# Performance work log

Measured on AMD Instinct MI355X. Metric: run time of the kernel, lower is better.

## Reference

```python
import jax, jax.numpy as jnp
import numpy as np

D_MODEL = 512
NUM_HEADS = 8
D_K = D_MODEL // NUM_HEADS  # 64
LN_EPS = 1e-5


def setup_inputs() -> dict:
    key = jax.random.key(0)
    ks = jax.random.split(key, 6)
    B, S, D = 8, 1024, D_MODEL
    scale = 1.0 / np.sqrt(D)
    return {
        "query": jax.random.normal(ks[0], (B, S, D), jnp.float32),
        "key": jax.random.normal(ks[1], (B, S, D), jnp.float32),
        "value": jax.random.normal(ks[2], (B, S, D), jnp.float32),
        "Wq": jax.random.normal(ks[3], (D, D), jnp.float32) * scale,
        "bq": jnp.zeros((D,), jnp.float32),
        "Wk": jax.random.normal(ks[4], (D, D), jnp.float32) * scale,
        "bk": jnp.zeros((D,), jnp.float32),
        "Wo": jax.random.normal(ks[5], (D, D * NUM_HEADS), jnp.float32) * (1.0 / np.sqrt(D * NUM_HEADS)),
        "bo": jnp.zeros((D,), jnp.float32),
        "gamma": jnp.ones((D,), jnp.float32),
        "beta": jnp.zeros((D,), jnp.float32),
    }


def reference(query, key, value, Wq, bq, Wk, bk, Wo, bo, gamma, beta):
    B, S, D = value.shape
    h, dk = NUM_HEADS, D_K
    # QK projections -> [B, h, S, dk]
    q = (query @ Wq.T + bq).reshape(B, S, h, dk).transpose(0, 2, 1, 3)
    k = (key @ Wk.T + bk).reshape(B, S, h, dk).transpose(0, 2, 1, 3)
    # scaled dot-product scores [B, h, Sq, Sk]
    scores = jnp.einsum("bhqd,bhkd->bhqk", q, k) / jnp.sqrt(jnp.asarray(dk, q.dtype))
    attn = jax.nn.softmax(scores, axis=-1)
    # value broadcast across heads: value is [B, Sk, D] -> per-head output [B, h, Sq, D]
    x = jnp.einsum("bhqk,bkd->bhqd", attn, value)
    # concat heads -> [B, Sq, h*D], output projection back to D
    x = x.transpose(0, 2, 1, 3).reshape(B, S, h * D)
    x = x @ Wo.T + bo
    # residual + LayerNorm (dropout = identity in eval)
    y = value + x
    mu = jnp.mean(y, axis=-1, keepdims=True)
    var = jnp.var(y, axis=-1, keepdims=True)
    out = (y - mu) * jax.lax.rsqrt(var + LN_EPS) * gamma + beta
    return out, attn
```

## Files before the change

kernel.cpp:

```cpp
#include <hip/hip_runtime.h>
#include <hip/hip_bf16.h>

#define B_ 8
#define S_ 1024
#define D_ 512
#define H_ 8
#define DK_ 64
#define HD_ 4096

typedef __attribute__((ext_vector_type(8))) short bf16x8;
typedef __attribute__((ext_vector_type(4))) float f32x4;

static __device__ __forceinline__ unsigned short f2bf(float f) {
    unsigned u = __float_as_uint(f);
    unsigned r = (u + 0x7fffu + ((u >> 16) & 1u)) >> 16;
    return (unsigned short)r;
}

static __device__ __forceinline__ void gload16(const unsigned short* g, unsigned short* l) {
    __builtin_amdgcn_global_load_lds(
        (const __attribute__((address_space(1))) void*)g,
        (__attribute__((address_space(3))) void*)l, 16, 0, 0);
}

static __device__ __forceinline__ int plidx(int ql, int k) {
    return ql * 1024 + ((((k >> 3) ^ (ql & 7))) << 3) + (k & 7);
}

__global__ __launch_bounds__(256) void cvt_kernel(
    const float* __restrict__ src, unsigned short* __restrict__ dst)
{
    const size_t i = ((size_t)blockIdx.x * 256 + threadIdx.x) * 4;
    float4 v = *(const float4*)&src[i];
    ushort4 u = { f2bf(v.x), f2bf(v.y), f2bf(v.z), f2bf(v.w) };
    *(ushort4*)&dst[i] = u;
}

__global__ __launch_bounds__(256) void vt_kernel(
    const float* __restrict__ V, unsigned short* __restrict__ Vt)
{
    __shared__ float tile[32][33];
    const int b = blockIdx.z, s0 = blockIdx.x * 32, e0 = blockIdx.y * 32;
    const int t = threadIdx.x;
    const int r = t >> 3, c4 = (t & 7) * 4;
    float4 v = *(const float4*)&V[((size_t)b * S_ + s0 + r) * D_ + e0 + c4];
    tile[r][c4 + 0] = v.x; tile[r][c4 + 1] = v.y;
    tile[r][c4 + 2] = v.z; tile[r][c4 + 3] = v.w;
    __syncthreads();
    ushort4 u;
    u.x = f2bf(tile[c4 + 0][r]); u.y = f2bf(tile[c4 + 1][r]);
    u.z = f2bf(tile[c4 + 2][r]); u.w = f2bf(tile[c4 + 3][r]);
    *(ushort4*)&Vt[((size_t)b * D_ + e0 + r) * S_ + s0 + c4] = u;
}

template<int KDIM, int MODE>
__global__ __launch_bounds__(256) void gemm128(
    const unsigned short* __restrict__ A, const unsigned short* __restrict__ Bw,
    const float* __restrict__ bias, const float* __restrict__ Vres,
    void* __restrict__ Out, float scale)
{
    const int o = blockIdx.x;
    const int nb = (o & 7) * 32 + (o >> 3);
    const int m0 = (nb >> 2) * 128;
    const int n0 = (nb & 3) * 128;

    __shared__ __align__(16) unsigned short As[2][128 * 32];
    __shared__ __align__(16) unsigned short Bs[2][128 * 32];

    const int t = threadIdx.x;
    const int wave = t >> 6, lane = t & 63;
    const int wr = wave >> 1, wc = wave & 1;
    const int lr = lane & 15, g = lane >> 4;
    const int gx = (g ^ (lr & 3)) << 3;

    f32x4 acc[4][4];
    #pragma unroll
    for (int r = 0; r < 4; ++r)
        #pragma unroll
        for (int c = 0; c < 4; ++c) acc[r][c] = (f32x4){0.f, 0.f, 0.f, 0.f};

    const int sub = lane >> 2;
    const int cb  = (((lane & 3) ^ (sub & 3)) << 3);

    auto stage = [&](int buf, int k0) {
        #pragma unroll
        for (int s = 0; s < 2; ++s) {
            const int chunk = s * 4 + wave;
            const int row = chunk * 16 + sub;
            gload16(&A [(size_t)(m0 + row) * KDIM + k0 + cb], &As[buf][chunk * 512]);
            gload16(&Bw[(size_t)(n0 + row) * KDIM + k0 + cb], &Bs[buf][chunk * 512]);
        }
    };
    auto compute = [&](int cur) {
        bf16x8 af[4], bfr[4];
        #pragma unroll
        for (int r = 0; r < 4; ++r)
            af[r] = *(const bf16x8*)&As[cur][(wr * 64 + r * 16 + lr) * 32 + gx];
        #pragma unroll
        for (int c = 0; c < 4; ++c)
            bfr[c] = *(const bf16x8*)&Bs[cur][(wc * 64 + c * 16 + lr) * 32 + gx];
        #pragma unroll
        for (int c = 0; c < 4; ++c)
            #pragma unroll
            for (int r = 0; r < 4; ++r)
                acc[r][c] = __builtin_amdgcn_mfma_f32_16x16x32_bf16(af[r], bfr[c], acc[r][c], 0, 0, 0);
    };

    const int NT = KDIM / 32;
    stage(0, 0);
    __syncthreads();
    int cur = 0;
    for (int tt = 0; tt < NT - 1; ++tt) {
        stage(cur ^ 1, (tt + 1) * 32);
        compute(cur);
        __syncthreads();
        cur ^= 1;
    }
    compute(cur);

    float bn[4];
    #pragma unroll
    for (int c = 0; c < 4; ++c) bn[c] = bias[n0 + wc * 64 + c * 16 + lr];

    #pragma unroll
    for (int r = 0; r < 4; ++r) {
        #pragma unroll
        for (int c = 0; c < 4; ++c) {
            const int n = n0 + wc * 64 + c * 16 + lr;
            #pragma unroll
            for (int i = 0; i < 4; ++i) {
                const int m = m0 + wr * 64 + r * 16 + g * 4 + i;
                if constexpr (MODE == 0) {
                    const int srow = m & 1023, bb = m >> 10;
                    const int h = n >> 6, dk = n & 63;
                    ((unsigned short*)Out)[(((size_t)(bb * H_ + h)) * S_ + srow) * DK_ + dk] =
                        f2bf((acc[r][c][i] + bn[c]) * scale);
                } else {
                    const size_t oo = (size_t)m * D_ + n;
                    ((float*)Out)[oo] = acc[r][c][i] + bn[c] + Vres[oo];
                }
            }
        }
    }
}

__global__ __launch_bounds__(1024, 4) void fused_attn(
    const unsigned short* __restrict__ Qbf,
    const unsigned short* __restrict__ Kbf,
    const unsigned short* __restrict__ Vt,
    float* __restrict__ attn,
    unsigned short* __restrict__ AV)
{
    const int bh = blockIdx.y;
    const int b = bh >> 3, h = bh & 7;
    const int q0 = blockIdx.x * 64;
    const unsigned short* Qb = Qbf + (size_t)bh * S_ * DK_;
    const unsigned short* Kb = Kbf + (size_t)bh * S_ * DK_;
    const unsigned short* Vb = Vt + (size_t)b * D_ * S_;
    float* outp = attn + ((size_t)bh << 20);

    __shared__ unsigned short PL[64 * 1024];
    __shared__ float redm[64][16];
    __shared__ float rowm[64];

    const int t = threadIdx.x;
    const int wave = t >> 6, lane = t & 63;
    const int wcol = wave * 64;
    const int lr = lane & 15;
    const int g  = lane >> 4;

    f32x4 acc[4][4];
    #pragma unroll
    for (int r = 0; r < 4; ++r)
        #pragma unroll
        for (int c = 0; c < 4; ++c) acc[r][c] = (f32x4){0.f, 0.f, 0.f, 0.f};

    #pragma unroll
    for (int kk = 0; kk < 2; ++kk) {
        bf16x8 af[4];
        #pragma unroll
        for (int r = 0; r < 4; ++r)
            af[r] = *(const bf16x8*)&Kb[(size_t)(wcol + r * 16 + lr) * DK_ + kk * 32 + g * 8];
        bf16x8 qf[4];
        #pragma unroll
        for (int c = 0; c < 4; ++c)
            qf[c] = *(const bf16x8*)&Qb[(size_t)(q0 + c * 16 + lr) * DK_ + kk * 32 + g * 8];
        #pragma unroll
        for (int r = 0; r < 4; ++r)
            #pragma unroll
            for (int c = 0; c < 4; ++c)
                acc[r][c] = __builtin_amdgcn_mfma_f32_16x16x32_bf16(af[r], qf[c], acc[r][c], 0, 0, 0);
    }

    float mloc[4];
    #pragma unroll
    for (int c = 0; c < 4; ++c) {
        float m = acc[0][c][0];
        #pragma unroll
        for (int r = 0; r < 4; ++r)
            #pragma unroll
            for (int i = 0; i < 4; ++i) m = fmaxf(m, acc[r][c][i]);
        m = fmaxf(m, __shfl_xor(m, 16));
        m = fmaxf(m, __shfl_xor(m, 32));
        mloc[c] = m;
    }
    if (lane < 16) {
        #pragma unroll
        for (int c = 0; c < 4; ++c) redm[c * 16 + lane][wave] = mloc[c];
    }
    __syncthreads();
    if (t < 64) {
        float m = redm[t][0];
        #pragma unroll
        for (int w = 1; w < 16; ++w) m = fmaxf(m, redm[t][w]);
        rowm[t] = m;
    }
    __syncthreads();
    float sloc[4];
    #pragma unroll
    for (int c = 0; c < 4; ++c) {
        const float m = rowm[c * 16 + lr];
        float s = 0.f;
        #pragma unroll
        for (int r = 0; r < 4; ++r)
            #pragma unroll
            for (int i = 0; i < 4; ++i) {
                float p = __expf(acc[r][c][i] - m);
                acc[r][c][i] = p;
                s += p;
            }
        s += __shfl_xor(s, 16);
        s += __shfl_xor(s, 32);
        sloc[c] = s;
    }
    if (lane < 16) {
        #pragma unroll
        for (int c = 0; c < 4; ++c) redm[c * 16 + lane][wave] = sloc[c];
    }
    __syncthreads();
    if (t < 64) {
        float s = redm[t][0];
        #pragma unroll
        for (int w = 1; w < 16; ++w) s += redm[t][w];
        rowm[t] = 1.0f / s;
    }
    __syncthreads();

    #pragma unroll
    for (int c = 0; c < 4; ++c) {
        const int ql = c * 16 + lr;
        const float ri = rowm[ql];
        #pragma unroll
        for (int r = 0; r < 4; ++r) {
            f32x4 v = acc[r][c];
            v[0] *= ri; v[1] *= ri; v[2] *= ri; v[3] *= ri;
            const int k = wcol + r * 16 + g * 4;
            unsigned p01 = (unsigned)f2bf(v[0]) | ((unsigned)f2bf(v[1]) << 16);
            unsigned p23 = (unsigned)f2bf(v[2]) | ((unsigned)f2bf(v[3]) << 16);
            uint2 pk = { p01, p23 };
            *(uint2*)&PL[plidx(ql, k)] = pk;
        }
    }
    __syncthreads();

    const int we = wave * 32;
    f32x4 accv[4][2];
    #pragma unroll
    for (int r = 0; r < 4; ++r)
        #pragma unroll
        for (int c = 0; c < 2; ++c) accv[r][c] = (f32x4){0.f, 0.f, 0.f, 0.f};

    for (int k0 = 0; k0 < S_; k0 += 32) {
        bf16x8 pa[4];
        #pragma unroll
        for (int r = 0; r < 4; ++r)
            pa[r] = *(const bf16x8*)&PL[plidx(r * 16 + lr, k0 + g * 8)];
        #pragma unroll
        for (int c = 0; c < 2; ++c) {
            const int e = we + c * 16 + lr;
            bf16x8 vf = *(const bf16x8*)&Vb[(size_t)e * S_ + k0 + g * 8];
            #pragma unroll
            for (int r = 0; r < 4; ++r)
                accv[r][c] = __builtin_amdgcn_mfma_f32_16x16x32_bf16(pa[r], vf, accv[r][c], 0, 0, 0);
        }
    }

    {
        const int arow = t >> 4;
        const int akb  = (t & 15) * 8;
        float* rowp = outp + ((size_t)(q0 + arow) << 10);
        #pragma unroll
        for (int j = 0; j < 8; ++j) {
            const int k = akb + j * 128;
            uint4 u = *(const uint4*)&PL[plidx(arow, k)];
            float4 f0, f1;
            f0.x = __uint_as_float((u.x & 0xffffu) << 16);
            f0.y = __uint_as_float(u.x & 0xffff0000u);
            f0.z = __uint_as_float((u.y & 0xffffu) << 16);
            f0.w = __uint_as_float(u.y & 0xffff0000u);
            f1.x = __uint_as_float((u.z & 0xffffu) << 16);
            f1.y = __uint_as_float(u.z & 0xffff0000u);
            f1.z = __uint_as_float((u.w & 0xffffu) << 16);
            f1.w = __uint_as_float(u.w & 0xffff0000u);
            *(float4*)&rowp[k] = f0;
            *(float4*)&rowp[k + 4] = f1;
        }
    }
    __syncthreads();

    unsigned short* PLs = PL;
    #pragma unroll
    for (int r = 0; r < 4; ++r)
        #pragma unroll
        for (int c = 0; c < 2; ++c) {
            const int e = we + c * 16 + lr;
            #pragma unroll
            for (int i = 0; i < 4; ++i) {
                const int q = r * 16 + g * 4 + i;
                PLs[q * 512 + (e ^ ((q & 7) << 3))] = f2bf(accv[r][c][i]);
            }
        }
    __syncthreads();
    {
        const int row = t >> 4;
        unsigned short* avp = AV + ((size_t)(b * S_ + q0 + row)) * HD_ + h * D_;
        #pragma unroll
        for (int j = 0; j < 4; ++j) {
            const int e0 = (t & 15) * 8 + j * 128;
            uint4 u = *(const uint4*)&PLs[row * 512 + (e0 ^ ((row & 7) << 3))];
            *(uint4*)&avp[e0] = u;
        }
    }
}

__global__ __launch_bounds__(256) void ln_kernel(
    float* __restrict__ Y, const float* __restrict__ gamma,
    const float* __restrict__ beta)
{
    const int lane = threadIdx.x & 63;
    const int wave = threadIdx.x >> 6;
    const size_t row = (size_t)blockIdx.x * 4 + wave;
    float* p = Y + row * D_;
    float4 v0 = *(float4*)&p[lane * 4];
    float4 v1 = *(float4*)&p[256 + lane * 4];
    float s = v0.x + v0.y + v0.z + v0.w + v1.x + v1.y + v1.z + v1.w;
    float q = v0.x * v0.x + v0.y * v0.y + v0.z * v0.z + v0.w * v0.w +
              v1.x * v1.x + v1.y * v1.y + v1.z * v1.z + v1.w * v1.w;
    #pragma unroll
    for (int m = 1; m < 64; m <<= 1) {
        s += __shfl_xor(s, m);
        q += __shfl_xor(q, m);
    }
    const float mu  = s * (1.f / 512.f);
    const float var = q * (1.f / 512.f) - mu * mu;
    const float r = rsqrtf(var + 1e-5f);
    const float4 g0 = *(const float4*)&gamma[lane * 4];
    const float4 g1 = *(const float4*)&gamma[256 + lane * 4];
    const float4 b0 = *(const float4*)&beta[lane * 4];
    const float4 b1 = *(const float4*)&beta[256 + lane * 4];
    v0.x = (v0.x - mu) * r * g0.x + b0.x;
    v0.y = (v0.y - mu) * r * g0.y + b0.y;
    v0.z = (v0.z - mu) * r * g0.z + b0.z;
    v0.w = (v0.w - mu) * r * g0.w + b0.w;
    v1.x = (v1.x - mu) * r * g1.x + b1.x;
    v1.y = (v1.y - mu) * r * g1.y + b1.y;
    v1.z = (v1.z - mu) * r * g1.z + b1.z;
    v1.w = (v1.w - mu) * r * g1.w + b1.w;
    *(float4*)&p[lane * 4] = v0;
    *(float4*)&p[256 + lane * 4] = v1;
}

extern "C" void kernel_launch(void* const* d_in, const int* in_sizes, int n_in,
                              void* d_out, int out_size, void* d_ws, size_t ws_size,
                              hipStream_t stream)
{
    const float* query = (const float*)d_in[0];
    const float* key   = (const float*)d_in[1];
    const float* value = (const float*)d_in[2];
    const float* Wq    = (const float*)d_in[3];
    const float* bq    = (const float*)d_in[4];
    const float* Wk    = (const float*)d_in[5];
    const float* bk    = (const float*)d_in[6];
    const float* Wo    = (const float*)d_in[7];
    const float* bo    = (const float*)d_in[8];
    const float* gamma = (const float*)d_in[9];
    const float* beta  = (const float*)d_in[10];

    float* out  = (float*)d_out;
    float* attn = out + (size_t)B_ * S_ * D_;
    char*  attnB = (char*)attn;

    char* ws = (char*)d_ws;
    unsigned short* AV   = (unsigned short*)ws;
    unsigned short* Vt   = (unsigned short*)(ws + ((size_t)64 << 20));
    unsigned short* Wobf = (unsigned short*)(ws + ((size_t)72 << 20));
    unsigned short* Qbf  = (unsigned short*)d_out;
    unsigned short* Kbf  = (unsigned short*)d_out + ((size_t)4 << 20);
    unsigned short* Xq   = (unsigned short*)(attnB + ((size_t)200 << 20));
    unsigned short* Xk   = (unsigned short*)(attnB + ((size_t)210 << 20));
    unsigned short* Wqbf = (unsigned short*)(attnB + ((size_t)220 << 20));
    unsigned short* Wkbf = (unsigned short*)(attnB + ((size_t)221 << 20));

    cvt_kernel<<<4096, 256, 0, stream>>>(query, Xq);
    cvt_kernel<<<4096, 256, 0, stream>>>(key,   Xk);
    cvt_kernel<<<256,  256, 0, stream>>>(Wq, Wqbf);
    cvt_kernel<<<256,  256, 0, stream>>>(Wk, Wkbf);
    cvt_kernel<<<2048, 256, 0, stream>>>(Wo, Wobf);
    vt_kernel<<<dim3(32, 16, 8), 256, 0, stream>>>(value, Vt);
    gemm128<512, 0><<<256, 256, 0, stream>>>(Xq, Wqbf, bq, nullptr, (void*)Qbf, 0.125f);
    gemm128<512, 0><<<256, 256, 0, stream>>>(Xk, Wkbf, bk, nullptr, (void*)Kbf, 1.0f);
    fused_attn<<<dim3(16, 64), 1024, 0, stream>>>(Qbf, Kbf, Vt, attn, AV);
    gemm128<4096, 1><<<256, 256, 0, stream>>>(AV, Wobf, bo, value, (void*)out, 0.f);
    ln_kernel<<<2048, 256, 0, stream>>>(out, gamma, beta);
}
```

Baseline: 396.6 us.

## Halve attention query tile, interleave attn writes with PV loop, narrow GEMM N-tiles

The fused attention kernel now handles 32 query rows per 512-thread block instead of 64 per 1024-thread block. This halves LDS use and should allow more blocks per CU. The fp32 attention-probability writeback is moved inside the PV MFMA loop so global stores overlap with compute, and the AV output is written straight from registers instead of being staged through LDS. The projection GEMMs are templated on N-tile width and use 128x64 tiles with 512 blocks for better CU coverage. The cost is less reuse of each V fragment load and AV stores that are scattered rather than coalesced.

After: 438.1 us. +10.5%, slower.

```diff
diff --git a/kernel.cpp b/kernel.cpp
--- a/kernel.cpp
+++ b/kernel.cpp
@@ -53,19 +53,22 @@
     *(ushort4*)&Vt[((size_t)b * D_ + e0 + r) * S_ + s0 + c4] = u;
 }
 
-template<int KDIM, int MODE>
-__global__ __launch_bounds__(256) void gemm128(
+template<int KDIM, int TN, int MODE>
+__global__ __launch_bounds__(256) void gemm_t(
     const unsigned short* __restrict__ A, const unsigned short* __restrict__ Bw,
     const float* __restrict__ bias, const float* __restrict__ Vres,
     void* __restrict__ Out, float scale)
 {
+    constexpr int NB = 512 / TN;
+    constexpr int CF = TN / 32;
     const int o = blockIdx.x;
-    const int nb = (o & 7) * 32 + (o >> 3);
-    const int m0 = (nb >> 2) * 128;
-    const int n0 = (nb & 3) * 128;
+    const int cpx = gridDim.x / 8;
+    const int nb = (o % 8) * cpx + o / 8;
+    const int m0 = (nb / NB) * 128;
+    const int n0 = (nb % NB) * TN;
 
     __shared__ __align__(16) unsigned short As[2][128 * 32];
-    __shared__ __align__(16) unsigned short Bs[2][128 * 32];
+    __shared__ __align__(16) unsigned short Bs[2][TN * 32];
 
     const int t = threadIdx.x;
     const int wave = t >> 6, lane = t & 63;
@@ -73,11 +76,11 @@
     const int lr = lane & 15, g = lane >> 4;
     const int gx = (g ^ (lr & 3)) << 3;
 
-    f32x4 acc[4][4];
+    f32x4 acc[4][CF];
     #pragma unroll
     for (int r = 0; r < 4; ++r)
         #pragma unroll
-        for (int c = 0; c < 4; ++c) acc[r][c] = (f32x4){0.f, 0.f, 0.f, 0.f};
+        for (int c = 0; c < CF; ++c) acc[r][c] = (f32x4){0.f, 0.f, 0.f, 0.f};
 
     const int sub = lane >> 2;
     const int cb  = (((lane & 3) ^ (sub & 3)) << 3);
@@ -87,20 +90,25 @@
         for (int s = 0; s < 2; ++s) {
             const int chunk = s * 4 + wave;
             const int row = chunk * 16 + sub;
-            gload16(&A [(size_t)(m0 + row) * KDIM + k0 + cb], &As[buf][chunk * 512]);
+            gload16(&A[(size_t)(m0 + row) * KDIM + k0 + cb], &As[buf][chunk * 512]);
+        }
+        #pragma unroll
+        for (int s = 0; s < TN / 64; ++s) {
+            const int chunk = s * 4 + wave;
+            const int row = chunk * 16 + sub;
             gload16(&Bw[(size_t)(n0 + row) * KDIM + k0 + cb], &Bs[buf][chunk * 512]);
         }
     };
     auto compute = [&](int cur) {
-        bf16x8 af[4], bfr[4];
+        bf16x8 af[4], bfr[CF];
         #pragma unroll
         for (int r = 0; r < 4; ++r)
             af[r] = *(const bf16x8*)&As[cur][(wr * 64 + r * 16 + lr) * 32 + gx];
         #pragma unroll
-        for (int c = 0; c < 4; ++c)
-            bfr[c] = *(const bf16x8*)&Bs[cur][(wc * 64 + c * 16 + lr) * 32 + gx];
-        #pragma unroll
-        for (int c = 0; c < 4; ++c)
+        for (int c = 0; c < CF; ++c)
+            bfr[c] = *(const bf16x8*)&Bs[cur][(wc * (TN / 2) + c * 16 + lr) * 32 + gx];
+        #pragma unroll
+        for (int c = 0; c < CF; ++c)
             #pragma unroll
             for (int r = 0; r < 4; ++r)
                 acc[r][c] = __builtin_amdgcn_mfma_f32_16x16x32_bf16(af[r], bfr[c], acc[r][c], 0, 0, 0);
@@ -118,15 +126,15 @@
     }
     compute(cur);
 
-    float bn[4];
-    #pragma unroll
-    for (int c = 0; c < 4; ++c) bn[c] = bias[n0 + wc * 64 + c * 16 + lr];
+    float bn[CF];
+    #pragma unroll
+    for (int c = 0; c < CF; ++c) bn[c] = bias[n0 + wc * (TN / 2) + c * 16 + lr];
 
     #pragma unroll
     for (int r = 0; r < 4; ++r) {
         #pragma unroll
-        for (int c = 0; c < 4; ++c) {
-            const int n = n0 + wc * 64 + c * 16 + lr;
+        for (int c = 0; c < CF; ++c) {
+            const int n = n0 + wc * (TN / 2) + c * 16 + lr;
             #pragma unroll
             for (int i = 0; i < 4; ++i) {
                 const int m = m0 + wr * 64 + r * 16 + g * 4 + i;
@@ -144,7 +152,7 @@
     }
 }
 
-__global__ __launch_bounds__(1024, 4) void fused_attn(
+__global__ __launch_bounds__(512, 4) void fused_attn(
     const unsigned short* __restrict__ Qbf,
     const unsigned short* __restrict__ Kbf,
     const unsigned short* __restrict__ Vt,
@@ -153,51 +161,55 @@
 {
     const int bh = blockIdx.y;
     const int b = bh >> 3, h = bh & 7;
-    const int q0 = blockIdx.x * 64;
+    const int q0 = blockIdx.x * 32;
     const unsigned short* Qb = Qbf + (size_t)bh * S_ * DK_;
     const unsigned short* Kb = Kbf + (size_t)bh * S_ * DK_;
     const unsigned short* Vb = Vt + (size_t)b * D_ * S_;
     float* outp = attn + ((size_t)bh << 20);
 
-    __shared__ unsigned short PL[64 * 1024];
-    __shared__ float redm[64][16];
-    __shared__ float rowm[64];
+    __shared__ unsigned short PL[32 * 1024];
+    __shared__ float redm[32][8];
+    __shared__ float rowm[32];
 
     const int t = threadIdx.x;
     const int wave = t >> 6, lane = t & 63;
-    const int wcol = wave * 64;
+    const int wcol = wave * 128;
     const int lr = lane & 15;
     const int g  = lane >> 4;
 
-    f32x4 acc[4][4];
-    #pragma unroll
-    for (int r = 0; r < 4; ++r)
-        #pragma unroll
-        for (int c = 0; c < 4; ++c) acc[r][c] = (f32x4){0.f, 0.f, 0.f, 0.f};
+    f32x4 acc[8][2];
+    #pragma unroll
+    for (int r = 0; r < 8; ++r)
+        #pragma unroll
+        for (int c = 0; c < 2; ++c) acc[r][c] = (f32x4){0.f, 0.f, 0.f, 0.f};
 
     #pragma unroll
     for (int kk = 0; kk < 2; ++kk) {
-        bf16x8 af[4];
-        #pragma unroll
-        for (int r = 0; r < 4; ++r)
-            af[r] = *(const bf16x8*)&Kb[(size_t)(wcol + r * 16 + lr) * DK_ + kk * 32 + g * 8];
-        bf16x8 qf[4];
-        #pragma unroll
-        for (int c = 0; c < 4; ++c)
+        bf16x8 qf[2];
+        #pragma unroll
+        for (int c = 0; c < 2; ++c)
             qf[c] = *(const bf16x8*)&Qb[(size_t)(q0 + c * 16 + lr) * DK_ + kk * 32 + g * 8];
         #pragma unroll
-        for (int r = 0; r < 4; ++r)
-            #pragma unroll
-            for (int c = 0; c < 4; ++c)
-                acc[r][c] = __builtin_amdgcn_mfma_f32_16x16x32_bf16(af[r], qf[c], acc[r][c], 0, 0, 0);
-    }
-
-    float mloc[4];
-    #pragma unroll
-    for (int c = 0; c < 4; ++c) {
+        for (int half = 0; half < 2; ++half) {
+            bf16x8 af[4];
+            #pragma unroll
+            for (int r = 0; r < 4; ++r)
+                af[r] = *(const bf16x8*)&Kb[(size_t)(wcol + (half * 4 + r) * 16 + lr) * DK_ + kk * 32 + g * 8];
+            #pragma unroll
+            for (int r = 0; r < 4; ++r)
+                #pragma unroll
+                for (int c = 0; c < 2; ++c)
+                    acc[half * 4 + r][c] =
+                        __builtin_amdgcn_mfma_f32_16x16x32_bf16(af[r], qf[c], acc[half * 4 + r][c], 0, 0, 0);
+        }
+    }
+
+    float mloc[2];
+    #pragma unroll
+    for (int c = 0; c < 2; ++c) {
         float m = acc[0][c][0];
         #pragma unroll
-        for (int r = 0; r < 4; ++r)
+        for (int r = 0; r < 8; ++r)
             #pragma unroll
             for (int i = 0; i < 4; ++i) m = fmaxf(m, acc[r][c][i]);
         m = fmaxf(m, __shfl_xor(m, 16));
@@ -206,23 +218,23 @@
     }
     if (lane < 16) {
         #pragma unroll
-        for (int c = 0; c < 4; ++c) redm[c * 16 + lane][wave] = mloc[c];
-    }
-    __syncthreads();
-    if (t < 64) {
+        for (int c = 0; c < 2; ++c) redm[c * 16 + lane][wave] = mloc[c];
+    }
+    __syncthreads();
+    if (t < 32) {
         float m = redm[t][0];
         #pragma unroll
-        for (int w = 1; w < 16; ++w) m = fmaxf(m, redm[t][w]);
+        for (int w = 1; w < 8; ++w) m = fmaxf(m, redm[t][w]);
         rowm[t] = m;
     }
     __syncthreads();
-    float sloc[4];
-    #pragma unroll
-    for (int c = 0; c < 4; ++c) {
+    float sloc[2];
+    #pragma unroll
+    for (int c = 0; c < 2; ++c) {
         const float m = rowm[c * 16 + lr];
         float s = 0.f;
         #pragma unroll
-        for (int r = 0; r < 4; ++r)
+        for (int r = 0; r < 8; ++r)
             #pragma unroll
             for (int i = 0; i < 4; ++i) {
                 float p = __expf(acc[r][c][i] - m);
@@ -233,25 +245,26 @@
         s += __shfl_xor(s, 32);
         sloc[c] = s;
     }
+    __syncthreads();
     if (lane < 16) {
         #pragma unroll
-        for (int c = 0; c < 4; ++c) redm[c * 16 + lane][wave] = sloc[c];
-    }
-    __syncthreads();
-    if (t < 64) {
+        for (int c = 0; c < 2; ++c) redm[c * 16 + lane][wave] = sloc[c];
+    }
+    __syncthreads();
+    if (t < 32) {
         float s = redm[t][0];
         #pragma unroll
-        for (int w = 1; w < 16; ++w) s += redm[t][w];
+        for (int w = 1; w < 8; ++w) s += redm[t][w];
         rowm[t] = 1.0f / s;
     }
     __syncthreads();
 
     #pragma unroll
-    for (int c = 0; c < 4; ++c) {
+    for (int c = 0; c < 2; ++c) {
         const int ql = c * 16 + lr;
         const float ri = rowm[ql];
         #pragma unroll
-        for (int r = 0; r < 4; ++r) {
+        for (int r = 0; r < 8; ++r) {
             f32x4 v = acc[r][c];
             v[0] *= ri; v[1] *= ri; v[2] *= ri; v[3] *= ri;
             const int k = wcol + r * 16 + g * 4;
@@ -263,72 +276,52 @@
     }
     __syncthreads();
 
-    const int we = wave * 32;
-    f32x4 accv[4][2];
-    #pragma unroll
-    for (int r = 0; r < 4; ++r)
-        #pragma unroll
-        for (int c = 0; c < 2; ++c) accv[r][c] = (f32x4){0.f, 0.f, 0.f, 0.f};
-
+    const int we = wave * 64;
+    f32x4 accv[2][4];
+    #pragma unroll
+    for (int r = 0; r < 2; ++r)
+        #pragma unroll
+        for (int c = 0; c < 4; ++c) accv[r][c] = (f32x4){0.f, 0.f, 0.f, 0.f};
+
+    const int arow = t >> 4;
+    const int acol = (t & 15) * 4;
+
+    #pragma unroll 2
     for (int k0 = 0; k0 < S_; k0 += 32) {
-        bf16x8 pa[4];
-        #pragma unroll
-        for (int r = 0; r < 4; ++r)
+        bf16x8 pa[2];
+        #pragma unroll
+        for (int r = 0; r < 2; ++r)
             pa[r] = *(const bf16x8*)&PL[plidx(r * 16 + lr, k0 + g * 8)];
-        #pragma unroll
-        for (int c = 0; c < 2; ++c) {
+        if ((k0 & 32) == 0) {
+            const int col = (k0 >> 6) * 64 + acol;
+            uint2 u = *(const uint2*)&PL[plidx(arow, col)];
+            float4 f;
+            f.x = __uint_as_float((u.x & 0xffffu) << 16);
+            f.y = __uint_as_float(u.x & 0xffff0000u);
+            f.z = __uint_as_float((u.y & 0xffffu) << 16);
+            f.w = __uint_as_float(u.y & 0xffff0000u);
+            *(float4*)&outp[((size_t)(q0 + arow) << 10) + col] = f;
+        }
+        #pragma unroll
+        for (int c = 0; c < 4; ++c) {
             const int e = we + c * 16 + lr;
             bf16x8 vf = *(const bf16x8*)&Vb[(size_t)e * S_ + k0 + g * 8];
             #pragma unroll
-            for (int r = 0; r < 4; ++r)
+            for (int r = 0; r < 2; ++r)
                 accv[r][c] = __builtin_amdgcn_mfma_f32_16x16x32_bf16(pa[r], vf, accv[r][c], 0, 0, 0);
         }
     }
 
-    {
-        const int arow = t >> 4;
-        const int akb  = (t & 15) * 8;
-        float* rowp = outp + ((size_t)(q0 + arow) << 10);
-        #pragma unroll
-        for (int j = 0; j < 8; ++j) {
-            const int k = akb + j * 128;
-            uint4 u = *(const uint4*)&PL[plidx(arow, k)];
-            float4 f0, f1;
-            f0.x = __uint_as_float((u.x & 0xffffu) << 16);
-            f0.y = __uint_as_float(u.x & 0xffff0000u);
-            f0.z = __uint_as_float((u.y & 0xffffu) << 16);
-            f0.w = __uint_as_float(u.y & 0xffff0000u);
-            f1.x = __uint_as_float((u.z & 0xffffu) << 16);
-            f1.y = __uint_as_float(u.z & 0xffff0000u);
-            f1.z = __uint_as_float((u.w & 0xffffu) << 16);
-            f1.w = __uint_as_float(u.w & 0xffff0000u);
-            *(float4*)&rowp[k] = f0;
-            *(float4*)&rowp[k + 4] = f1;
-        }
-    }
-    __syncthreads();
-
-    unsigned short* PLs = PL;
-    #pragma unroll
-    for (int r = 0; r < 4; ++r)
-        #pragma unroll
-        for (int c = 0; c < 2; ++c) {
+    #pragma unroll
+    for (int r = 0; r < 2; ++r) {
+        #pragma unroll
+        for (int c = 0; c < 4; ++c) {
             const int e = we + c * 16 + lr;
             #pragma unroll
             for (int i = 0; i < 4; ++i) {
-                const int q = r * 16 + g * 4 + i;
-                PLs[q * 512 + (e ^ ((q & 7) << 3))] = f2bf(accv[r][c][i]);
+                const int row = q0 + r * 16 + g * 4 + i;
+                AV[((size_t)(b * S_ + row)) * HD_ + h * D_ + e] = f2bf(accv[r][c][i]);
             }
-        }
-    __syncthreads();
-    {
-        const int row = t >> 4;
-        unsigned short* avp = AV + ((size_t)(b * S_ + q0 + row)) * HD_ + h * D_;
-        #pragma unroll
-        for (int j = 0; j < 4; ++j) {
-            const int e0 = (t & 15) * 8 + j * 128;
-            uint4 u = *(const uint4*)&PLs[row * 512 + (e0 ^ ((row & 7) << 3))];
-            *(uint4*)&avp[e0] = u;
         }
     }
 }
@@ -407,9 +400,9 @@
     cvt_kernel<<<256,  256, 0, stream>>>(Wk, Wkbf);
     cvt_kernel<<<2048, 256, 0, stream>>>(Wo, Wobf);
     vt_kernel<<<dim3(32, 16, 8), 256, 0, stream>>>(value, Vt);
-    gemm128<512, 0><<<256, 256, 0, stream>>>(Xq, Wqbf, bq, nullptr, (void*)Qbf, 0.125f);
-    gemm128<512, 0><<<256, 256, 0, stream>>>(Xk, Wkbf, bk, nullptr, (void*)Kbf, 1.0f);
-    fused_attn<<<dim3(16, 64), 1024, 0, stream>>>(Qbf, Kbf, Vt, attn, AV);
-    gemm128<4096, 1><<<256, 256, 0, stream>>>(AV, Wobf, bo, value, (void*)out, 0.f);
+    gemm_t<512, 64, 0><<<512, 256, 0, stream>>>(Xq, Wqbf, bq, nullptr, (void*)Qbf, 0.125f);
+    gemm_t<512, 64, 0><<<512, 256, 0, stream>>>(Xk, Wkbf, bk, nullptr, (void*)Kbf, 1.0f);
+    fused_attn<<<dim3(32, 64), 512, 0, stream>>>(Qbf, Kbf, Vt, attn, AV);
+    gemm_t<4096, 64, 1><<<512, 256, 0, stream>>>(AV, Wobf, bo, value, (void*)out, 0.f);
     ln_kernel<<<2048, 256, 0, stream>>>(out, gamma, beta);
 }
```
